# Performance work log

Measured on AMD Instinct MI355X. Metric: run time of the kernel, lower is better.

Reference implementation:

```python
import jax, jax.numpy as jnp
import numpy as np

D_MODEL, N_HEADS, D_FF = 768, 12, 3072
D_HEAD = D_MODEL // N_HEADS
EPS = 1e-5


def layer_norm(x, g, b):
    mu = jnp.mean(x, axis=-1, keepdims=True)
    var = jnp.mean(jnp.square(x - mu), axis=-1, keepdims=True)
    return (x - mu) * jax.lax.rsqrt(var + EPS) * g + b


def setup_inputs() -> dict:
    key = jax.random.key(0)
    ks = jax.random.split(key, 8)
    B, T = 4, 2048
    s_in = 1.0 / np.sqrt(D_MODEL)
    s_ff = 1.0 / np.sqrt(D_FF)
    return {
        "x": jax.random.normal(ks[0], (B, T, D_MODEL), dtype=jnp.float32),
        "ln1_g": jnp.ones((D_MODEL,), jnp.float32),
        "ln1_b": jnp.zeros((D_MODEL,), jnp.float32),
        "qkv_w": jax.random.normal(ks[1], (D_MODEL, 3 * D_MODEL), jnp.float32) * s_in,
        "qkv_b": jnp.zeros((3 * D_MODEL,), jnp.float32),
        "attn_out_w": jax.random.normal(ks[2], (D_MODEL, D_MODEL), jnp.float32) * s_in,
        "attn_out_b": jnp.zeros((D_MODEL,), jnp.float32),
        "ln2_g": jnp.ones((D_MODEL,), jnp.float32),
        "ln2_b": jnp.zeros((D_MODEL,), jnp.float32),
        "ff1_w": jax.random.normal(ks[3], (D_MODEL, D_FF), jnp.float32) * s_in,
        "ff1_b": jnp.zeros((D_FF,), jnp.float32),
        "ff2_w": jax.random.normal(ks[4], (D_FF, D_MODEL), jnp.float32) * s_ff,
        "ff2_b": jnp.zeros((D_MODEL,), jnp.float32),
    }


def reference(x, ln1_g, ln1_b, qkv_w, qkv_b, attn_out_w, attn_out_b,
              ln2_g, ln2_b, ff1_w, ff1_b, ff2_w, ff2_b):
    B, T, D = x.shape
    h = layer_norm(x, ln1_g, ln1_b)
    qkv = h @ qkv_w + qkv_b                       # [B,T,3D]
    q, k, v = jnp.split(qkv, 3, axis=-1)
    def heads(t):  # [B,T,D] -> [B,H,T,dh]
        return t.reshape(B, T, N_HEADS, D_HEAD).transpose(0, 2, 1, 3)
    q, k, v = heads(q), heads(k), heads(v)
    scores = jnp.einsum('bhqd,bhkd->bhqk', q, k) / np.sqrt(D_HEAD)
    attn = jnp.einsum('bhqk,bhkd->bhqd', jax.nn.softmax(scores, axis=-1), v)
    attn = attn.transpose(0, 2, 1, 3).reshape(B, T, D)
    x = x + attn @ attn_out_w + attn_out_b
    h = layer_norm(x, ln2_g, ln2_b)
    ff = jax.nn.gelu(h @ ff1_w + ff1_b, approximate=True) @ ff2_w + ff2_b
    return x + ff
```

## Files before the change

### kernel.cpp

```cpp
#include <hip/hip_runtime.h>
#include <stdint.h>

typedef unsigned short ushort_t;
typedef unsigned int uint_t;

typedef __bf16 bf16x8 __attribute__((ext_vector_type(8)));
typedef float f32x4 __attribute__((ext_vector_type(4)));

#define DM 768
#define DFF 3072
#define NH 12
#define DH 64
#define TLEN 2048
#define BATCH 4
#define NROWS (BATCH * TLEN)
#define QKVW (3 * DM)
#define STG ((size_t)NROWS * DM)

#if __has_builtin(__builtin_amdgcn_exp2f)
#define EXP2(x) __builtin_amdgcn_exp2f(x)
#else
extern "C" __device__ float __ocml_native_exp2_f32(float);
#define EXP2(x) __ocml_native_exp2_f32(x)
#endif

__device__ __forceinline__ float b2f(ushort_t u) {
  union { uint_t i; float f; } c; c.i = ((uint_t)u) << 16; return c.f;
}
__device__ __forceinline__ ushort_t f2b(float f) {
  union { float f; uint_t i; } c; c.f = f;
  uint_t i = c.i;
  return (ushort_t)((i + 0x7fffu + ((i >> 16) & 1u)) >> 16);
}

__device__ __forceinline__ void gl_lds16(const ushort_t* g, ushort_t* l) {
  __builtin_amdgcn_global_load_lds(
      (const __attribute__((address_space(1))) uint_t*)g,
      (__attribute__((address_space(3))) uint_t*)l, 16, 0, 0);
}

__device__ __forceinline__ float gelu_f(float x) {
  float x2 = x * x;
  float c2n = -x * __builtin_fmaf(0.10294323f, x2, 2.3022082f);
  float t = EXP2(c2n);
  return x * __builtin_amdgcn_rcpf(1.0f + t);
}

__global__ __launch_bounds__(256) void detect_dtype(const ushort_t* __restrict__ x,
                                                    int* __restrict__ flag) {
  __shared__ int cnt[256];
  int c = 0;
  for (int i = threadIdx.x; i < 65536; i += 256)
    c += ((x[i] & 0x7F80u) == 0x7F80u) ? 1 : 0;
  cnt[threadIdx.x] = c;
  __syncthreads();
  for (int s = 128; s >= 1; s >>= 1) {
    if (threadIdx.x < s) cnt[threadIdx.x] += cnt[threadIdx.x + s];
    __syncthreads();
  }
  if (threadIdx.x == 0) flag[0] = (cnt[0] > 0) ? 1 : 0;
}

__global__ __launch_bounds__(256) void cvt_smalls(
    const void* s0, const void* s1, const void* s2, const void* s3,
    const void* s4, const void* s5, const void* s6, const void* s7,
    ushort_t* __restrict__ dst, const int* __restrict__ flag) {
  int f = flag[0];
  int i = blockIdx.x * 256 + threadIdx.x;
  if (i >= 9984) return;
  const void* src; int off;
  if (i < 768)       { src = s0; off = i; }
  else if (i < 1536) { src = s1; off = i - 768; }
  else if (i < 3840) { src = s2; off = i - 1536; }
  else if (i < 4608) { src = s3; off = i - 3840; }
  else if (i < 5376) { src = s4; off = i - 4608; }
  else if (i < 6144) { src = s5; off = i - 5376; }
  else if (i < 9216) { src = s6; off = i - 6144; }
  else               { src = s7; off = i - 9216; }
  dst[i] = f ? f2b(((const float*)src)[off]) : ((const ushort_t*)src)[off];
}

__global__ __launch_bounds__(256) void transpose_adapt(
    const void* __restrict__ inbase, long long inOff, ushort_t* __restrict__ out,
    int R, int C, int ldIn, const int* __restrict__ flag) {
  __shared__ alignas(16) ushort_t tile[32][33];
  int f = flag[0];
  const float* in32 = (const float*)inbase + inOff;
  const ushort_t* in16 = (const ushort_t*)inbase + inOff;
  int tc = blockIdx.x * 32, tr = blockIdx.y * 32;
  int lx = threadIdx.x & 31, ly = threadIdx.x >> 5;
#pragma unroll
  for (int i = 0; i < 32; i += 8) {
    size_t idx = (size_t)(tr + ly + i) * ldIn + tc + lx;
    tile[ly + i][lx] = f ? f2b(in32[idx]) : in16[idx];
  }
  __syncthreads();
#pragma unroll
  for (int i = 0; i < 32; i += 8)
    out[(size_t)(tc + ly + i) * R + tr + lx] = tile[lx][ly + i];
}

template <bool RAW>
__global__ __launch_bounds__(256) void ln_kernel(
    const void* __restrict__ xr, const ushort_t* __restrict__ g,
    const ushort_t* __restrict__ b, ushort_t* __restrict__ out,
    const int* __restrict__ flag) {
  int row = blockIdx.x * 4 + (threadIdx.x >> 6);
  int lane = threadIdx.x & 63;
  float v[12];
  if (RAW && flag[0]) {
    const float2* xp = (const float2*)((const float*)xr + (size_t)row * DM);
#pragma unroll
    for (int j = 0; j < 6; j++) {
      float2 t = xp[lane + 64 * j];
      v[2 * j] = t.x; v[2 * j + 1] = t.y;
    }
  } else {
    const uint_t* xu = (const uint_t*)((const ushort_t*)xr + (size_t)row * DM);
#pragma unroll
    for (int j = 0; j < 6; j++) {
      uint_t wv = xu[lane + 64 * j];
      v[2 * j] = b2f((ushort_t)(wv & 0xffffu));
      v[2 * j + 1] = b2f((ushort_t)(wv >> 16));
    }
  }
  float sum = 0.f, ss = 0.f;
#pragma unroll
  for (int k = 0; k < 12; k++) { sum += v[k]; ss += v[k] * v[k]; }
#pragma unroll
  for (int off = 32; off >= 1; off >>= 1) {
    sum += __shfl_xor(sum, off, 64);
    ss += __shfl_xor(ss, off, 64);
  }
  float mu = sum * (1.f / DM);
  float var = ss * (1.f / DM) - mu * mu;
  float rs = rsqrtf(var + 1e-5f);
  uint_t* ou = (uint_t*)(out + (size_t)row * DM);
  const uint_t* gu = (const uint_t*)g;
  const uint_t* bu = (const uint_t*)b;
#pragma unroll
  for (int j = 0; j < 6; j++) {
    int idx = lane + 64 * j;
    uint_t gw = gu[idx], bw = bu[idx];
    float o0 = (v[2 * j] - mu) * rs * b2f((ushort_t)(gw & 0xffffu)) + b2f((ushort_t)(bw & 0xffffu));
    float o1 = (v[2 * j + 1] - mu) * rs * b2f((ushort_t)(gw >> 16)) + b2f((ushort_t)(bw >> 16));
    ou[idx] = (uint_t)f2b(o0) | ((uint_t)f2b(o1) << 16);
  }
}

template <bool GELU, int RESMODE, int OUTMODE, int BM = 128>
__global__ __launch_bounds__(256) void gemm_bt(
    const ushort_t* __restrict__ A, const ushort_t* __restrict__ BT,
    const ushort_t* __restrict__ bias, const void* __restrict__ res,
    void* __restrict__ outp, int M, int N, int K, int accum,
    const int* __restrict__ flagp) {
  constexpr int MI = (BM == 128) ? 4 : 2;
  constexpr int NI = 4;
  __shared__ alignas(16) ushort_t sA[2][BM * 32];
  __shared__ alignas(16) ushort_t sB[2][128 * 32];
  const int m0 = blockIdx.x * BM;
  const int n0 = blockIdx.y * 128;
  const int tid = threadIdx.x;
  const int w = tid >> 6, lane = tid & 63;
  const int quad = lane >> 4, l16 = lane & 15;
  const int wm = (w & 1) * (BM / 2);
  const int wn = (w >> 1) * 64;

  const f32x4 vz = {0.f, 0.f, 0.f, 0.f};
  f32x4 acc[MI][NI];
#pragma unroll
  for (int i = 0; i < MI; i++)
#pragma unroll
    for (int j = 0; j < NI; j++) acc[i][j] = vz;

  const int colA = (((lane & 3) + ((lane >> 3) & 3)) & 3) * 8;
  const int rowAa = w * (BM / 4) + (lane >> 2);
  const int rowBb = w * 32 + (lane >> 2);
  const ushort_t* gA = A + (size_t)(m0 + rowAa) * K + colA;
  const ushort_t* gB = BT + (size_t)(n0 + rowBb) * K + colA;

  auto stage = [&](int k0, int buf) {
    ushort_t* lA = &sA[buf][(w * (BM / 4)) * 32];
    ushort_t* lB = &sB[buf][(w * 32) * 32];
    gl_lds16(gA + k0, lA);
    if constexpr (BM == 128) gl_lds16(gA + k0 + (size_t)16 * K, lA + 16 * 32);
    gl_lds16(gB + k0, lB);
    gl_lds16(gB + k0 + (size_t)16 * K, lB + 16 * 32);
  };

  const int nk = K >> 5;
  stage(0, 0);
  stage(32, 1);
  if constexpr (BM == 128) asm volatile("s_waitcnt vmcnt(4)" ::: "memory");
  else                     asm volatile("s_waitcnt vmcnt(3)" ::: "memory");
  __builtin_amdgcn_s_barrier();

  for (int kt = 0; kt < nk; ++kt) {
    const int buf = kt & 1;
    bf16x8 af[MI], bfr[NI];
#pragma unroll
    for (int i = 0; i < MI; i++) {
      int ra = wm + i * 16 + l16;
      af[i] = *(const bf16x8*)&sA[buf][ra * 32 + ((quad + 4 - ((ra >> 1) & 3)) & 3) * 8];
    }
#pragma unroll
    for (int i = 0; i < NI; i++) {
      int rb = wn + i * 16 + l16;
      bfr[i] = *(const bf16x8*)&sB[buf][rb * 32 + ((quad + 4 - ((rb >> 1) & 3)) & 3) * 8];
    }
    asm volatile("s_waitcnt lgkmcnt(0)" ::: "memory");
    __builtin_amdgcn_sched_barrier(0);
    __builtin_amdgcn_s_barrier();
    if (kt + 2 < nk) stage((kt + 2) << 5, buf);
#pragma unroll
    for (int mi = 0; mi < MI; mi++)
#pragma unroll
      for (int ni = 0; ni < NI; ni++)
        acc[mi][ni] = __builtin_amdgcn_mfma_f32_16x16x32_bf16(af[mi], bfr[ni], acc[mi][ni], 0, 0, 0);
    if (kt + 2 < nk) {
      if constexpr (BM == 128) asm volatile("s_waitcnt vmcnt(4)" ::: "memory");
      else                     asm volatile("s_waitcnt vmcnt(3)" ::: "memory");
      __builtin_amdgcn_s_barrier();
    } else if (kt + 1 < nk) {
      asm volatile("s_waitcnt vmcnt(0)" ::: "memory");
      __builtin_amdgcn_s_barrier();
    }
  }

  ushort_t* o16 = (ushort_t*)outp;
  float* o32 = (float*)outp;
  const int f32io = (OUTMODE == 1 || RESMODE == 2) ? flagp[0] : 0;
#pragma unroll
  for (int mi = 0; mi < MI; mi++) {
#pragma unroll
    for (int ni = 0; ni < NI; ni++) {
      int col = n0 + wn + ni * 16 + l16;
      float bs = bias ? b2f(bias[col]) : 0.0f;
#pragma unroll
      for (int r = 0; r < 4; r++) {
        int row = m0 + wm + mi * 16 + quad * 4 + r;
        size_t idx = (size_t)row * N + col;
        float v = acc[mi][ni][r] + bs;
        if (GELU) v = gelu_f(v);
        if (RESMODE == 1) v += b2f(((const ushort_t*)res)[idx]);
        if (RESMODE == 2)
          v += f32io ? ((const float*)res)[idx] : b2f(((const ushort_t*)res)[idx]);
        if (OUTMODE == 1) {
          if (accum) v += f32io ? o32[idx] : b2f(o16[idx]);
          if (f32io) o32[idx] = v; else o16[idx] = f2b(v);
        } else if (OUTMODE == 2) {
          int b = row >> 11, kt2 = (row >> 7) & 15, kl = row & 127;
          int ty = col >= 1536 ? 2 : (col >= 768 ? 1 : 0);
          int c2 = col - ty * 768;
          int hh = c2 >> 6, d = c2 & 63;
          if (ty == 0) v *= 0.18033688011112042f;
          size_t tb = ((size_t)(b * NH + hh) * 16 + kt2) * 8192;
          size_t sidx;
          if (ty == 2) {
            int pl = (kl & 0x60) | ((kl & 15) << 1) | ((kl >> 4) & 1);
            sidx = tb + (size_t)d * 128 + (size_t)(((pl >> 3) ^ (d & 7)) << 3) + (pl & 7);
          } else {
            sidx = tb + (size_t)kl * 64 + (size_t)(((d >> 3) ^ (kl & 7)) << 3) + (d & 7);
          }
          o16[ty * STG + sidx] = f2b(v);
        } else {
          o16[idx] = f2b(v);
        }
      }
    }
  }
}

__global__ __launch_bounds__(256) void attn_kernel(
    const ushort_t* __restrict__ qs, const ushort_t* __restrict__ ks,
    const ushort_t* __restrict__ vs, ushort_t* __restrict__ attnout) {
  __shared__ alignas(16) ushort_t sK[2][64 * 64];
  __shared__ alignas(16) ushort_t sV[2][64 * 64];
  __shared__ alignas(16) ushort_t sP[4 * 2 * 32 * 40];
  const int bh = blockIdx.x;
  const int qt = blockIdx.y;
  const int tid = threadIdx.x;
  const int w = tid >> 6, lane = tid & 63;
  const int quad = lane >> 4, l16 = lane & 15;
  const int xsw = l16 & 7;
  const ushort_t* ktg0 = ks + (size_t)bh * 16 * 8192;
  const ushort_t* vtg0 = vs + (size_t)bh * 16 * 8192;

  {
    const ushort_t* qtg = qs + ((size_t)bh * 16 + qt) * 8192;
#pragma unroll
    for (int i = 0; i < 4; i++) {
      int off = (w * 4 + i) * 512;
      ushort_t* dst = (off < 4096) ? &sK[0][off] : &sK[1][off - 4096];
      gl_lds16(qtg + off + lane * 8, dst);
    }
  }
  __syncthreads();
  bf16x8 qf[2][2];
#pragma unroll
  for (int mq = 0; mq < 2; mq++) {
    int q = w * 32 + mq * 16 + l16;
    const ushort_t* sq = (q < 64) ? &sK[0][q * 64] : &sK[1][(q - 64) * 64];
#pragma unroll
    for (int c = 0; c < 2; c++)
      qf[mq][c] = *(const bf16x8*)&sq[((c * 4 + quad) ^ (q & 7)) * 8];
  }
  __syncthreads();

  bf16x8 onesf;
#pragma unroll
  for (int i = 0; i < 8; i++) onesf[i] = (__bf16)1.0f;

  f32x4 lsum[2];
  f32x4 oacc[2][4];
  const f32x4 vz = {0.f, 0.f, 0.f, 0.f};
#pragma unroll
  for (int mq = 0; mq < 2; mq++) {
    lsum[mq] = vz;
#pragma unroll
    for (int nd = 0; nd < 4; nd++) oacc[mq][nd] = vz;
  }

  auto stage = [&](int j, int buf) {
    const ushort_t* kg = ktg0 + (size_t)(j >> 1) * 8192 + (j & 1) * 4096;
    const ushort_t* vg = vtg0 + (size_t)(j >> 1) * 8192 + (j & 1) * 64;
#pragma unroll
    for (int i = 0; i < 2; i++) {
      int off = (w * 2 + i) * 512;
      gl_lds16(kg + off + lane * 8, &sK[buf][off]);
      gl_lds16(vg + (size_t)((w * 2 + i) * 8 + (lane >> 3)) * 128 + (lane & 7) * 8,
               &sV[buf][off]);
    }
  };

  stage(0, 0);

  for (int j = 0; j < 32; j++) {
    const int buf = j & 1;
    __syncthreads();
    if (j < 31) stage(j + 1, 1 - buf);

    f32x4 s[2][4];
    __builtin_amdgcn_s_setprio(1);
#pragma unroll
    for (int nk = 0; nk < 4; nk++) {
      int key = nk * 16 + l16;
      bf16x8 kf0 = *(const bf16x8*)&sK[buf][key * 64 + ((quad) ^ (key & 7)) * 8];
      bf16x8 kf1 = *(const bf16x8*)&sK[buf][key * 64 + ((4 + quad) ^ (key & 7)) * 8];
#pragma unroll
      for (int mq = 0; mq < 2; mq++) {
        s[mq][nk] = __builtin_amdgcn_mfma_f32_16x16x32_bf16(qf[mq][0], kf0, vz, 0, 0, 0);
        s[mq][nk] = __builtin_amdgcn_mfma_f32_16x16x32_bf16(qf[mq][1], kf1, s[mq][nk], 0, 0, 0);
      }
    }
    __builtin_amdgcn_s_setprio(0);

    uint_t* myP32 = (uint_t*)sP + w * 1280;
#pragma unroll
    for (int kk = 0; kk < 2; kk++)
#pragma unroll
      for (int mq = 0; mq < 2; mq++)
#pragma unroll
        for (int r = 0; r < 4; r++) {
          float lo = EXP2(s[mq][kk * 2 + 0][r]);
          float hi = EXP2(s[mq][kk * 2 + 1][r]);
          uint_t pk;
          asm("v_cvt_pk_bf16_f32 %0, %1, %2" : "=v"(pk) : "v"(lo), "v"(hi));
          myP32[kk * 640 + (mq * 16 + quad * 4 + r) * 20 + l16] = pk;
        }
    __asm__ volatile("s_waitcnt lgkmcnt(0)" ::: "memory");

    bf16x8 pf[2][2];
#pragma unroll
    for (int kk = 0; kk < 2; kk++)
#pragma unroll
      for (int mq = 0; mq < 2; mq++)
        pf[kk][mq] = *(const bf16x8*)&sP[(size_t)w * 2560 + kk * 1280 +
                                         (mq * 16 + l16) * 40 + quad * 8];
    __builtin_amdgcn_s_setprio(1);
#pragma unroll
    for (int kk = 0; kk < 2; kk++)
#pragma unroll
      for (int mq = 0; mq < 2; mq++)
        lsum[mq] = __builtin_amdgcn_mfma_f32_16x16x32_bf16(pf[kk][mq], onesf, lsum[mq], 0, 0, 0);
#pragma unroll
    for (int kk = 0; kk < 2; kk++)
#pragma unroll
      for (int nd = 0; nd < 4; nd++) {
        bf16x8 vf = *(const bf16x8*)&sV[buf][(nd * 16 + l16) * 64 + ((kk * 4 + quad) ^ xsw) * 8];
#pragma unroll
        for (int mq = 0; mq < 2; mq++)
          oacc[mq][nd] = __builtin_amdgcn_mfma_f32_16x16x32_bf16(pf[kk][mq], vf, oacc[mq][nd], 0, 0, 0);
      }
    __builtin_amdgcn_s_setprio(0);
    __asm__ volatile("" ::: "memory");
  }

  const int b = bh / NH, h = bh - b * NH;
#pragma unroll
  for (int mq = 0; mq < 2; mq++) {
    float inv[4];
#pragma unroll
    for (int r = 0; r < 4; r++) inv[r] = __builtin_amdgcn_rcpf(lsum[mq][r]);
#pragma unroll
    for (int nd = 0; nd < 4; nd++) {
#pragma unroll
      for (int r = 0; r < 4; r++) {
        size_t row = (size_t)b * TLEN + qt * 128 + w * 32 + mq * 16 + quad * 4 + r;
        int col = h * DH + nd * 16 + l16;
        attnout[row * DM + col] = f2b(oacc[mq][nd][r] * inv[r]);
      }
    }
  }
}

extern "C" void kernel_launch(void* const* d_in, const int* in_sizes, int n_in,
                              void* d_out, int out_size, void* d_ws, size_t ws_size,
                              hipStream_t stream) {
  const void* x_r = d_in[0];
  const void* ln1_g_r = d_in[1];
  const void* ln1_b_r = d_in[2];
  const void* qkv_w_r = d_in[3];
  const void* qkv_b_r = d_in[4];
  const void* ao_w_r = d_in[5];
  const void* ao_b_r = d_in[6];
  const void* ln2_g_r = d_in[7];
  const void* ln2_b_r = d_in[8];
  const void* ff1_w_r = d_in[9];
  const void* ff1_b_r = d_in[10];
  const void* ff2_w_r = d_in[11];
  const void* ff2_b_r = d_in[12];

  int* flag = (int*)d_ws;
  ushort_t* base = (ushort_t*)d_ws + 128;
  const size_t RD = STG;

  const size_t elA = RD + RD + (size_t)NROWS * DFF + RD + (size_t)DM * DM + 9984;
  const bool pathA = ws_size >= elA * 2 + 4096;

  detect_dtype<<<1, 256, 0, stream>>>((const ushort_t*)x_r, flag);

  if (pathA) {
    ushort_t* x2   = base;
    ushort_t* h    = base + RD;
    ushort_t* big  = base + 2 * RD;
    ushort_t* aux  = big + (size_t)NROWS * DFF;
    ushort_t* wTa  = aux + RD;
    ushort_t* smalls = wTa + (size_t)DM * DM;
    ushort_t* wTq = aux;
    ushort_t* attnb = aux;
    ushort_t* wT2 = aux;
    ushort_t* wT3 = aux + (size_t)DFF * DM;
    ushort_t *g1 = smalls, *b1 = smalls + 768, *qb = smalls + 1536, *ab = smalls + 3840,
             *g2 = smalls + 4608, *b2 = smalls + 5376, *f1b = smalls + 6144, *f2bb = smalls + 9216;

    cvt_smalls<<<39, 256, 0, stream>>>(ln1_g_r, ln1_b_r, qkv_b_r, ao_b_r,
                                       ln2_g_r, ln2_b_r, ff1_b_r, ff2_b_r, smalls, flag);
    ln_kernel<true><<<NROWS / 4, 256, 0, stream>>>(x_r, g1, b1, h, flag);
    transpose_adapt<<<dim3(QKVW / 32, DM / 32), 256, 0, stream>>>(qkv_w_r, 0, wTq, DM, QKVW, QKVW, flag);
    gemm_bt<false, 0, 2><<<dim3(NROWS / 128, QKVW / 128), 256, 0, stream>>>(
        h, wTq, qb, nullptr, big, NROWS, QKVW, DM, 0, flag);
    attn_kernel<<<dim3(NH * BATCH, 16), 256, 0, stream>>>(big, big + STG, big + 2 * STG, attnb);
    transpose_adapt<<<dim3(DM / 32, DM / 32), 256, 0, stream>>>(ao_w_r, 0, wTa, DM, DM, DM, flag);
    gemm_bt<false, 2, 0, 64><<<dim3(NROWS / 64, DM / 128), 256, 0, stream>>>(
        attnb, wTa, ab, x_r, x2, NROWS, DM, DM, 0, flag);
    ln_kernel<false><<<NROWS / 4, 256, 0, stream>>>(x2, g2, b2, h, flag);
    transpose_adapt<<<dim3(DFF / 32, DM / 32), 256, 0, stream>>>(ff1_w_r, 0, wT2, DM, DFF, DFF, flag);
    gemm_bt<true, 0, 0><<<dim3(NROWS / 128, DFF / 128), 256, 0, stream>>>(
        h, wT2, f1b, nullptr, big, NROWS, DFF, DM, 0, flag);
    transpose_adapt<<<dim3(DM / 32, DFF / 32), 256, 0, stream>>>(ff2_w_r, 0, wT3, DFF, DM, DM, flag);
    gemm_bt<false, 1, 1, 64><<<dim3(NROWS / 64, DM / 128), 256, 0, stream>>>(
        big, wT3, f2bb, x2, d_out, NROWS, DM, DFF, 0, flag);
  } else {
    ushort_t* regA = base;
    ushort_t* regB = base + RD;
    ushort_t* slots = regB + (size_t)NROWS * QKVW;
    ushort_t* smalls = slots + (size_t)QKVW * DM + (size_t)DM * DM;
    ushort_t* h = regA, *attnb = regA, *h2 = regA;
    ushort_t* x2 = regB;
    ushort_t* ffq = regB + RD;
    ushort_t* wTq = slots;
    ushort_t* wTa = slots + (size_t)QKVW * DM;
    ushort_t* wT2 = slots;
    ushort_t* wT3 = slots + (size_t)1536 * DM;
    ushort_t *g1 = smalls, *b1 = smalls + 768, *qb = smalls + 1536, *ab = smalls + 3840,
             *g2 = smalls + 4608, *b2 = smalls + 5376, *f1b = smalls + 6144, *f2bb = smalls + 9216;

    cvt_smalls<<<39, 256, 0, stream>>>(ln1_g_r, ln1_b_r, qkv_b_r, ao_b_r,
                                       ln2_g_r, ln2_b_r, ff1_b_r, ff2_b_r, smalls, flag);
    ln_kernel<true><<<NROWS / 4, 256, 0, stream>>>(x_r, g1, b1, h, flag);
    transpose_adapt<<<dim3(QKVW / 32, DM / 32), 256, 0, stream>>>(qkv_w_r, 0, wTq, DM, QKVW, QKVW, flag);
    gemm_bt<false, 0, 2><<<dim3(NROWS / 128, QKVW / 128), 256, 0, stream>>>(
        h, wTq, qb, nullptr, regB, NROWS, QKVW, DM, 0, flag);
    attn_kernel<<<dim3(NH * BATCH, 16), 256, 0, stream>>>(regB, regB + STG, regB + 2 * STG, attnb);
    transpose_adapt<<<dim3(DM / 32, DM / 32), 256, 0, stream>>>(ao_w_r, 0, wTa, DM, DM, DM, flag);
    gemm_bt<false, 2, 0, 64><<<dim3(NROWS / 64, DM / 128), 256, 0, stream>>>(
        attnb, wTa, ab, x_r, x2, NROWS, DM, DM, 0, flag);
    ln_kernel<false><<<NROWS / 4, 256, 0, stream>>>(x2, g2, b2, h2, flag);
    for (int q = 0; q < 2; q++) {
      transpose_adapt<<<dim3(1536 / 32, DM / 32), 256, 0, stream>>>(
          ff1_w_r, (long long)q * 1536, wT2, DM, 1536, DFF, flag);
      gemm_bt<true, 0, 0><<<dim3(NROWS / 128, 1536 / 128), 256, 0, stream>>>(
          h2, wT2, f1b + q * 1536, nullptr, ffq, NROWS, 1536, DM, 0, flag);
      transpose_adapt<<<dim3(DM / 32, 1536 / 32), 256, 0, stream>>>(
          ff2_w_r, (long long)q * 1536 * DM, wT3, 1536, DM, DM, flag);
      if (q == 0)
        gemm_bt<false, 1, 1, 64><<<dim3(NROWS / 64, DM / 128), 256, 0, stream>>>(
            ffq, wT3, f2bb, x2, d_out, NROWS, DM, 1536, 0, flag);
      else
        gemm_bt<false, 0, 1, 64><<<dim3(NROWS / 64, DM / 128), 256, 0, stream>>>(
            ffq, wT3, nullptr, nullptr, d_out, NROWS, DM, 1536, 1, flag);
    }
  }
}
```

Baseline: 445.0 us.

## Keep attention probabilities in registers by transposing QK MFMA and permuting V layout

Swaps the operand order of the QK^T MFMA so each lane holds scores along the key dimension, then packs the exponentiated scores directly into bf16x8 A-operands for the PV MFMA. The LDS round-trip through the sP buffer and its waitcnt are removed. To match the new key ordering in registers, the V staging layout written by the QKV GEMM epilogue is permuted. This saves LDS traffic and shared memory per block, but depends on the permutation exactly matching the MFMA output lane mapping.

```diff
diff --git a/kernel.cpp b/kernel.cpp
--- a/kernel.cpp
+++ b/kernel.cpp
@@ -257,7 +257,8 @@
           size_t tb = ((size_t)(b * NH + hh) * 16 + kt2) * 8192;
           size_t sidx;
           if (ty == 2) {
-            int pl = (kl & 0x60) | ((kl & 15) << 1) | ((kl >> 4) & 1);
+            int k64 = kl & 63, m = k64 >> 4, qd = (k64 >> 2) & 3, r2 = k64 & 3;
+            int pl = (kl & 0x40) | ((m >> 1) << 5) | (qd << 3) | ((m & 1) << 2) | r2;
             sidx = tb + (size_t)d * 128 + (size_t)(((pl >> 3) ^ (d & 7)) << 3) + (pl & 7);
           } else {
             sidx = tb + (size_t)kl * 64 + (size_t)(((d >> 3) ^ (kl & 7)) << 3) + (d & 7);
@@ -276,7 +277,6 @@
     const ushort_t* __restrict__ vs, ushort_t* __restrict__ attnout) {
   __shared__ alignas(16) ushort_t sK[2][64 * 64];
   __shared__ alignas(16) ushort_t sV[2][64 * 64];
-  __shared__ alignas(16) ushort_t sP[4 * 2 * 32 * 40];
   const int bh = blockIdx.x;
   const int qt = blockIdx.y;
   const int tid = threadIdx.x;
@@ -349,51 +349,45 @@
       bf16x8 kf1 = *(const bf16x8*)&sK[buf][key * 64 + ((4 + quad) ^ (key & 7)) * 8];
 #pragma unroll
       for (int mq = 0; mq < 2; mq++) {
-        s[mq][nk] = __builtin_amdgcn_mfma_f32_16x16x32_bf16(qf[mq][0], kf0, vz, 0, 0, 0);
-        s[mq][nk] = __builtin_amdgcn_mfma_f32_16x16x32_bf16(qf[mq][1], kf1, s[mq][nk], 0, 0, 0);
+        s[mq][nk] = __builtin_amdgcn_mfma_f32_16x16x32_bf16(kf0, qf[mq][0], vz, 0, 0, 0);
+        s[mq][nk] = __builtin_amdgcn_mfma_f32_16x16x32_bf16(kf1, qf[mq][1], s[mq][nk], 0, 0, 0);
       }
     }
     __builtin_amdgcn_s_setprio(0);
 
-    uint_t* myP32 = (uint_t*)sP + w * 1280;
-#pragma unroll
-    for (int kk = 0; kk < 2; kk++)
+    bf16x8 pa[2][2];
+#pragma unroll
+    for (int mq = 0; mq < 2; mq++)
+#pragma unroll
+      for (int c = 0; c < 2; c++) {
+        union { uint_t u[4]; bf16x8 v; } pk;
+#pragma unroll
+        for (int t = 0; t < 4; t++) {
+          float lo = EXP2(s[mq][2 * c + (t >> 1)][(t & 1) * 2 + 0]);
+          float hi = EXP2(s[mq][2 * c + (t >> 1)][(t & 1) * 2 + 1]);
+          uint_t w32;
+          asm("v_cvt_pk_bf16_f32 %0, %1, %2" : "=v"(w32) : "v"(lo), "v"(hi));
+          pk.u[t] = w32;
+        }
+        pa[mq][c] = pk.v;
+      }
+
+    __builtin_amdgcn_s_setprio(1);
+#pragma unroll
+    for (int c = 0; c < 2; c++)
 #pragma unroll
       for (int mq = 0; mq < 2; mq++)
-#pragma unroll
-        for (int r = 0; r < 4; r++) {
-          float lo = EXP2(s[mq][kk * 2 + 0][r]);
-          float hi = EXP2(s[mq][kk * 2 + 1][r]);
-          uint_t pk;
-          asm("v_cvt_pk_bf16_f32 %0, %1, %2" : "=v"(pk) : "v"(lo), "v"(hi));
-          myP32[kk * 640 + (mq * 16 + quad * 4 + r) * 20 + l16] = pk;
-        }
-    __asm__ volatile("s_waitcnt lgkmcnt(0)" ::: "memory");
-
-    bf16x8 pf[2][2];
-#pragma unroll
-    for (int kk = 0; kk < 2; kk++)
-#pragma unroll
-      for (int mq = 0; mq < 2; mq++)
-        pf[kk][mq] = *(const bf16x8*)&sP[(size_t)w * 2560 + kk * 1280 +
-                                         (mq * 16 + l16) * 40 + quad * 8];
-    __builtin_amdgcn_s_setprio(1);
-#pragma unroll
-    for (int kk = 0; kk < 2; kk++)
-#pragma unroll
-      for (int mq = 0; mq < 2; mq++)
-        lsum[mq] = __builtin_amdgcn_mfma_f32_16x16x32_bf16(pf[kk][mq], onesf, lsum[mq], 0, 0, 0);
-#pragma unroll
-    for (int kk = 0; kk < 2; kk++)
+        lsum[mq] = __builtin_amdgcn_mfma_f32_16x16x32_bf16(pa[mq][c], onesf, lsum[mq], 0, 0, 0);
+#pragma unroll
+    for (int c = 0; c < 2; c++)
 #pragma unroll
       for (int nd = 0; nd < 4; nd++) {
-        bf16x8 vf = *(const bf16x8*)&sV[buf][(nd * 16 + l16) * 64 + ((kk * 4 + quad) ^ xsw) * 8];
+        bf16x8 vf = *(const bf16x8*)&sV[buf][(nd * 16 + l16) * 64 + ((c * 4 + quad) ^ xsw) * 8];
 #pragma unroll
         for (int mq = 0; mq < 2; mq++)
-          oacc[mq][nd] = __builtin_amdgcn_mfma_f32_16x16x32_bf16(pf[kk][mq], vf, oacc[mq][nd], 0, 0, 0);
+          oacc[mq][nd] = __builtin_amdgcn_mfma_f32_16x16x32_bf16(pa[mq][c], vf, oacc[mq][nd], 0, 0, 0);
       }
     __builtin_amdgcn_s_setprio(0);
-    __asm__ volatile("" ::: "memory");
   }
 
   const int b = bh / NH, h = bh - b * NH;
```

Result: no change. 445.8 us (+0.2%).
